# Performance work log

Hardware: AMD Instinct MI355X
Metric: run time of the kernel (lower is better)

The kernel has to match this reference:

```python
import jax, jax.numpy as jnp
import numpy as np
from jax import lax

B, CIN, H, W = 16, 96, 112, 112
C1, C2 = CIN * 2, CIN * 4          # 192, 384 (t1=(2,2))
SQ = 24                            # make_divisible(96//4, 4)
EPS = 1e-5


def _conv(x, w, stride, pad, groups):
    return lax.conv_general_dilated(
        x, w, window_strides=stride, padding=pad,
        feature_group_count=groups,
        dimension_numbers=("NCHW", "OIHW", "NCHW"))


def _bn(x, g, b, m, v):
    scale = (g / jnp.sqrt(v + EPS))[None, :, None, None]
    return (x - m[None, :, None, None]) * scale + b[None, :, None, None]


def _shuffle(x, groups):
    b, c, h, w = x.shape
    return x.reshape(b, groups, c // groups, h, w).transpose(0, 2, 1, 3, 4).reshape(b, c, h, w)


# DYShiftMax channel permutation for g=1: rotate channels left by 1
_DY_IDX = np.roll(np.arange(CIN), -1)


def setup_inputs() -> dict:
    key = jax.random.key(0)
    ks = jax.random.split(key, 16)
    f32 = jnp.float32
    d = {}
    d["x"] = jax.random.normal(ks[0], (B, CIN, H, W), f32)
    # depthwise (k,1) conv, groups=CIN, multiplier 2
    d["w_dw1"] = jax.random.normal(ks[1], (C1, 1, 3, 1), f32) * 0.2
    d["bn1_g"] = jax.random.uniform(ks[2], (C1,), f32, 0.5, 1.5)
    d["bn1_b"] = jax.random.normal(ks[3], (C1,), f32) * 0.1
    d["bn1_m"] = jax.random.normal(ks[4], (C1,), f32) * 0.1
    d["bn1_v"] = jax.random.uniform(ks[5], (C1,), f32, 0.5, 1.5)
    # depthwise (1,k) conv, groups=C1, multiplier 2
    d["w_dw2"] = jax.random.normal(ks[6], (C2, 1, 1, 3), f32) * 0.2
    d["bn2_g"] = jax.random.uniform(ks[7], (C2,), f32, 0.5, 1.5)
    d["bn2_b"] = jax.random.normal(ks[8], (C2,), f32) * 0.1
    d["bn2_m"] = jax.random.normal(ks[9], (C2,), f32) * 0.1
    d["bn2_v"] = jax.random.uniform(ks[10], (C2,), f32, 0.5, 1.5)
    # 1x1 pointwise conv 384 -> 96 (ConvModule, bias-free conv + BN, identity act)
    d["w_pw"] = jax.random.normal(ks[11], (CIN, C2, 1, 1), f32) * (1.0 / np.sqrt(C2))
    d["bn3_g"] = jax.random.uniform(ks[12], (CIN,), f32, 0.5, 1.5)
    d["bn3_b"] = jax.random.normal(ks[13], (CIN,), f32) * 0.1
    d["bn3_m"] = jax.random.normal(ks[14], (CIN,), f32) * 0.1
    d["bn3_v"] = jax.random.uniform(ks[15], (CIN,), f32, 0.5, 1.5)
    # DYShiftMax squeeze-excite FC: CIN -> SQ -> 2*CIN (exp=2)
    k2 = jax.random.split(jax.random.fold_in(key, 1), 4)
    d["fc1_w"] = jax.random.normal(k2[0], (SQ, CIN), f32) * (1.0 / np.sqrt(CIN))
    d["fc1_b"] = jax.random.normal(k2[1], (SQ,), f32) * 0.1
    d["fc2_w"] = jax.random.normal(k2[2], (2 * CIN, SQ), f32) * (1.0 / np.sqrt(SQ))
    d["fc2_b"] = jax.random.normal(k2[3], (2 * CIN,), f32) * 0.1
    return d


def reference(x, w_dw1, bn1_g, bn1_b, bn1_m, bn1_v,
              w_dw2, bn2_g, bn2_b, bn2_m, bn2_v,
              w_pw, bn3_g, bn3_b, bn3_m, bn3_v,
              fc1_w, fc1_b, fc2_w, fc2_b):
    # DepthSpatialSepConv: depthwise (3,1) then depthwise (1,3), each + BN
    h = _conv(x, w_dw1, (1, 1), ((1, 1), (0, 0)), groups=CIN)
    h = _bn(h, bn1_g, bn1_b, bn1_m, bn1_v)
    h = _conv(h, w_dw2, (1, 1), ((0, 0), (1, 1)), groups=C1)
    h = _bn(h, bn2_g, bn2_b, bn2_m, bn2_v)
    # ReLU6 (y2 == 0)
    h = jnp.clip(h, 0.0, 6.0)
    # ChannelShuffle(6)
    h = _shuffle(h, 6)
    # 1x1 ConvModule (groups=1, identity activation) + BN
    h = _conv(h, w_pw, (1, 1), ((0, 0), (0, 0)), groups=1)
    h = _bn(h, bn3_g, bn3_b, bn3_m, bn3_v)
    # DYShiftMax(out, out, (1,0), (0,0), act_relu=False -> exp=2, g=1)
    y = h.mean(axis=(2, 3))                       # [B, CIN] global avg pool
    y = jnp.maximum(y @ fc1_w.T + fc1_b, 0.0)     # Linear + ReLU
    y = y @ fc2_w.T + fc2_b                       # Linear -> [B, 2*CIN]
    y = jnp.clip(y + 3.0, 0.0, 6.0) / 6.0         # HSigmoid
    y = (y - 0.5) * 4.0
    a1 = y[:, :CIN] + 1.0                         # init_a[0] = 1.0
    b1 = y[:, CIN:]                               # init_b[0] = 0.0
    h2 = h[:, _DY_IDX, :, :]                      # shifted channels
    h = h * a1[:, :, None, None] + h2 * b1[:, :, None, None]
    # ChannelShuffle(g2=1) is identity; ChannelShuffle(out//2)
    h = _shuffle(h, CIN // 2)
    # residual (stride==1 and in==out)
    return h + x
```

## Files before the change

### kernel.cpp

```cpp
#include <hip/hip_runtime.h>
#include <hip/hip_bf16.h>

#define BATCH 16
#define CINC 96
#define HGT 112
#define WID 112
#define HW 12544
#define C1N 192
#define C2N 384
#define EPSV 1e-5f

typedef _Float16 f16x8 __attribute__((ext_vector_type(8)));
typedef _Float16 f16x4 __attribute__((ext_vector_type(4)));
typedef float    f32x4 __attribute__((ext_vector_type(4)));

#define WS_S      0
#define WS_A1B1   1536
#define WS_W1F    4608
#define WS_B1F    5184
#define WS_W2F    5376
#define WS_B2F    6528
#define WS_S3     6912
#define WS_B3     7008
#define WS_WPF_BYTES (7104*4)
#define WS_H_BYTES   (WS_WPF_BYTES + CINC*C2N*2)

__global__ void k_prep(const float* __restrict__ wdw1, const float* __restrict__ g1,
                       const float* __restrict__ bb1, const float* __restrict__ m1,
                       const float* __restrict__ v1,
                       const float* __restrict__ wdw2, const float* __restrict__ g2,
                       const float* __restrict__ bb2, const float* __restrict__ m2,
                       const float* __restrict__ v2,
                       const float* __restrict__ wpw, const float* __restrict__ g3,
                       const float* __restrict__ bb3, const float* __restrict__ m3,
                       const float* __restrict__ v3,
                       float* ws)
{
    int t = blockIdx.x * blockDim.x + threadIdx.x;
    int stride = gridDim.x * blockDim.x;
    float* w1f = ws + WS_W1F; float* b1f = ws + WS_B1F;
    float* w2f = ws + WS_W2F; float* b2f = ws + WS_B2F;
    float* s3  = ws + WS_S3;  float* b3f = ws + WS_B3;
    _Float16* wpf = (_Float16*)((char*)ws + WS_WPF_BYTES);

    for (int c = t; c < C1N; c += stride) {
        float s = g1[c] / sqrtf(v1[c] + EPSV);
        w1f[c*3+0] = wdw1[c*3+0] * s;
        w1f[c*3+1] = wdw1[c*3+1] * s;
        w1f[c*3+2] = wdw1[c*3+2] * s;
        b1f[c] = bb1[c] - m1[c] * s;
    }
    for (int c = t; c < C2N; c += stride) {
        float s = g2[c] / sqrtf(v2[c] + EPSV);
        w2f[c*3+0] = wdw2[c*3+0] * s;
        w2f[c*3+1] = wdw2[c*3+1] * s;
        w2f[c*3+2] = wdw2[c*3+2] * s;
        b2f[c] = bb2[c] - m2[c] * s;
    }
    for (int c = t; c < CINC; c += stride) {
        float s = g3[c] / sqrtf(v3[c] + EPSV);
        s3[c] = s; b3f[c] = bb3[c] - m3[c] * s;
    }
    for (int idx = t; idx < CINC * C2N; idx += stride) {
        int e = idx & 7;
        int l2 = idx >> 3;
        int lane = l2 & 63;
        int l3 = l2 >> 6;
        int rt = l3 % 6, ksg = l3 / 6;
        int m = rt * 16 + (lane & 15);
        int k = ksg * 32 + (lane >> 4) * 8 + e;
        int o = (k & 63) * 6 + (k >> 6);
        wpf[idx] = (_Float16)wpw[m * C2N + o];
    }
}

__global__ __launch_bounds__(256, 3) void k_main6(const float* __restrict__ x,
                                                  const float* __restrict__ ws,
                                                  float* __restrict__ sums,
                                                  _Float16* __restrict__ h_out)
{
    __shared__ __align__(16) char u_raw[256 * 208];
    __shared__ float ssum[CINC];

    int t   = threadIdx.x;
    int bid = blockIdx.x;
    int logical = (bid & 7) * 112 + (bid >> 3);
    int b   = logical / 56;
    int rem = logical - b * 56;
    int y0  = (rem >> 1) * 4;
    int x0  = (rem & 1) * 48;

    int wv = t >> 6, lane = t & 63;
    int r = lane >> 4, c4 = lane & 15;
    int gy = y0 + r;
    int gc = x0 + 4 * c4;
    int col16 = c4, g = r;

    const float* w1f = ws + WS_W1F; const float* b1f = ws + WS_B1F;
    const float* w2f = ws + WS_W2F; const float* b2f = ws + WS_B2F;

    if (t < CINC) ssum[t] = 0.f;

    bool ymok = gy >= 1;
    bool ypok = gy + 1 < HGT;
    bool isE  = (c4 == 0) | (c4 == 15);
    int  ecol = (c4 == 0) ? (x0 - 1) : (x0 + 64);
    bool ev   = isE && ((unsigned)ecol < (unsigned)WID);
    int  secol = ev ? ecol : 0;
    int  tm = ymok ? -WID : 0;
    int  tp = ypok ?  WID : 0;

    f32x4 acc[6][4];
    #pragma unroll
    for (int rt = 0; rt < 6; ++rt)
        #pragma unroll
        for (int ct = 0; ct < 4; ++ct) acc[rt][ct] = (f32x4){0.f, 0.f, 0.f, 0.f};

    const f16x8* wpf_g = (const f16x8*)((const char*)ws + WS_WPF_BYTES);
    long xb = (long)b * CINC * HW;
    long rowoff = (long)gy * WID;

    int rotbase = 3 * r + c4;
    char* ub0 = u_raw + (r * 64 + 4 * c4) * 208;

    for (int chunk = 0; chunk < 4; ++chunk) {
        if (chunk) __syncthreads();

        f16x4 uvbuf[4];
        #pragma unroll
        for (int i = 0; i < 6; ++i) {
            int cl = wv * 6 + i;
            int cu = __builtin_amdgcn_readfirstlane(chunk * 24 + cl);
            const float* xc = x + xb + (long)cu * HW;
            const float* xp = xc + rowoff + gc;
            f32x4 mid = *(const f32x4*)xp;
            f32x4 top = *(const f32x4*)(xp + tm);
            f32x4 bot = *(const f32x4*)(xp + tp);

            float eT = 0.f, eM = 0.f, eB = 0.f;
            if (isE) {
                const float* ep = xc + rowoff + secol;
                eM = ep[0];
                eT = ep[tm];
                eB = ep[tp];
            }

            int c1a = cu * 2;
            float wa0 = w1f[c1a*3+0], wa1 = w1f[c1a*3+1], wa2 = w1f[c1a*3+2], ba = b1f[c1a];
            float wb0 = w1f[c1a*3+3], wb1 = w1f[c1a*3+4], wb2 = w1f[c1a*3+5], bb = b1f[c1a+1];

            float va[4], vb[4];
            #pragma unroll
            for (int j = 0; j < 4; ++j) {
                float tt = ymok ? top[j] : 0.f;
                float bt = ypok ? bot[j] : 0.f;
                va[j] = fmaf(wa0, tt, fmaf(wa1, mid[j], fmaf(wa2, bt, ba)));
                vb[j] = fmaf(wb0, tt, fmaf(wb1, mid[j], fmaf(wb2, bt, bb)));
            }
            float etS = (ymok && ev) ? eT : 0.f;
            float ebS = (ypok && ev) ? eB : 0.f;
            float emS = ev ? eM : 0.f;
            float vea = ev ? fmaf(wa0, etS, fmaf(wa1, emS, fmaf(wa2, ebS, ba))) : 0.f;
            float veb = ev ? fmaf(wb0, etS, fmaf(wb1, emS, fmaf(wb2, ebS, bb))) : 0.f;

            float vLa = __shfl(va[3], (lane + 63) & 63);
            float vLb = __shfl(vb[3], (lane + 63) & 63);
            float vRa = __shfl(va[0], (lane + 1) & 63);
            float vRb = __shfl(vb[0], (lane + 1) & 63);
            if (c4 == 0)  { vLa = vea; vLb = veb; }
            if (c4 == 15) { vRa = vea; vRb = veb; }

            int c2b = cu * 4;
            float w20[4], w21[4], w22[4], b2v[4];
            #pragma unroll
            for (int jj = 0; jj < 4; ++jj) {
                w20[jj] = w2f[(c2b+jj)*3+0];
                w21[jj] = w2f[(c2b+jj)*3+1];
                w22[jj] = w2f[(c2b+jj)*3+2];
                b2v[jj] = b2f[c2b+jj];
            }

            float pa[6] = {vLa, va[0], va[1], va[2], va[3], vRa};
            float pb[6] = {vLb, vb[0], vb[1], vb[2], vb[3], vRb};

            f16x4 uv[4];
            #pragma unroll
            for (int j = 0; j < 4; ++j) {
                #pragma unroll
                for (int jj = 0; jj < 4; ++jj) {
                    float p0 = (jj < 2) ? pa[j]     : pb[j];
                    float p1 = (jj < 2) ? pa[j + 1] : pb[j + 1];
                    float p2 = (jj < 2) ? pa[j + 2] : pb[j + 2];
                    float tv = fmaf(w20[jj], p0, fmaf(w21[jj], p1, fmaf(w22[jj], p2, b2v[jj])));
                    tv = fminf(fmaxf(tv, 0.f), 6.f);
                    uv[j][jj] = (_Float16)tv;
                }
            }

            if ((i & 1) == 0) {
                #pragma unroll
                for (int j = 0; j < 4; ++j) uvbuf[j] = uv[j];
            } else {
                int slot = ((cl >> 1) + rotbase) % 12;
                char* ubase = ub0 + slot * 16;
                #pragma unroll
                for (int j = 0; j < 4; ++j) {
                    f16x8 w = __builtin_shufflevector(uvbuf[j], uv[j], 0, 1, 2, 3, 4, 5, 6, 7);
                    *(f16x8*)(ubase + j * 208) = w;
                }
            }
        }
        __syncthreads();

        #pragma unroll
        for (int ks = 0; ks < 3; ++ks) {
            f16x8 bfr[4];
            #pragma unroll
            for (int ct = 0; ct < 4; ++ct) {
                int pos = wv * 64 + ct * 16 + col16;
                int sl = (ks * 4 + g + 3 * wv + ((pos >> 2) & 15)) % 12;
                bfr[ct] = *(const f16x8*)(u_raw + pos * 208 + sl * 16);
            }
            #pragma unroll
            for (int rt = 0; rt < 6; ++rt) {
                f16x8 afr = wpf_g[((chunk * 3 + ks) * 6 + rt) * 64 + lane];
                #pragma unroll
                for (int ct = 0; ct < 4; ++ct)
                    acc[rt][ct] = __builtin_amdgcn_mfma_f32_16x16x32_f16(afr, bfr[ct], acc[rt][ct], 0, 0, 0);
            }
        }
    }
    __syncthreads();

    _Float16* h_s = (_Float16*)u_raw;
    const float* s3  = ws + WS_S3;
    const float* b3f = ws + WS_B3;
    #pragma unroll
    for (int rt = 0; rt < 6; ++rt) {
        #pragma unroll
        for (int ct = 0; ct < 4; ++ct) {
            int p = wv * 64 + ct * 16 + col16;
            #pragma unroll
            for (int rr = 0; rr < 4; ++rr) {
                int m = rt * 16 + g * 4 + rr;
                h_s[m * 264 + p] = (_Float16)fmaf(acc[rt][ct][rr], s3[m], b3f[m]);
            }
        }
    }
    __syncthreads();

    #pragma unroll
    for (int i = 0; i < 12; ++i) {
        int flat = i * 2048 + t * 8;
        int m = flat >> 8;
        int p = flat & 255;
        f16x8 hv = *(const f16x8*)(h_s + m * 264 + p);
        int row = y0 + (p >> 6);
        int colg = x0 + (p & 63);
        *(f16x8*)(h_out + ((long)(b * CINC + m)) * HW + (long)row * WID + colg) = hv;

        float s = 0.f;
        if (!(x0 == 48 && (p & 63) < 16)) {
            #pragma unroll
            for (int e = 0; e < 8; ++e) s += (float)hv[e];
        }
        s += __shfl_xor(s, 1);
        s += __shfl_xor(s, 2);
        s += __shfl_xor(s, 4);
        s += __shfl_xor(s, 8);
        s += __shfl_xor(s, 16);
        if ((lane & 31) == 0) atomicAdd(&ssum[m], s);
    }
    __syncthreads();
    if (t < CINC) atomicAdd(&sums[b * CINC + t], ssum[t]);
}

__global__ __launch_bounds__(192) void k_gates(const float* __restrict__ sums,
                                               const float* __restrict__ fc1w,
                                               const float* __restrict__ fc1b,
                                               const float* __restrict__ fc2w,
                                               const float* __restrict__ fc2b,
                                               float* __restrict__ a1b1)
{
    __shared__ float mean_s[CINC];
    __shared__ float mid[24];
    int b = blockIdx.x;
    int t = threadIdx.x;

    if (t < CINC) mean_s[t] = sums[b * CINC + t] * (1.0f / 12544.0f);
    __syncthreads();
    if (t < 24) {
        float d = fc1b[t];
        #pragma unroll 4
        for (int c = 0; c < CINC; ++c) d = fmaf(fc1w[t * CINC + c], mean_s[c], d);
        mid[t] = fmaxf(d, 0.f);
    }
    __syncthreads();
    {
        float d = fc2b[t];
        #pragma unroll
        for (int j = 0; j < 24; ++j) d = fmaf(fc2w[t * 24 + j], mid[j], d);
        float y = fminf(fmaxf(d + 3.f, 0.f), 6.f) * (1.f / 6.f);
        y = (y - 0.5f) * 4.f;
        a1b1[b * 192 + t] = (t < CINC) ? (y + 1.f) : y;
    }
}

__global__ __launch_bounds__(256) void k_final(const _Float16* __restrict__ h,
                                               const float* __restrict__ xin,
                                               const float* __restrict__ a1b1,
                                               float* __restrict__ out)
{
    int q = blockIdx.x * 256 + threadIdx.x;
    int pos4 = q % 3136;
    int bo = q / 3136;
    int o = bo % CINC, b = bo / CINC;
    int c = (o % 48) * 2 + (o / 48);
    int cn = (c + 1) % CINC;

    float av = a1b1[b * 192 + c];
    float bv = a1b1[b * 192 + 96 + c];

    long hb = (long)b * CINC * HW;
    f16x4 hv4 = *(const f16x4*)(h + hb + (long)c  * HW + pos4 * 4);
    f16x4 h2v = *(const f16x4*)(h + hb + (long)cn * HW + pos4 * 4);

    long xo = ((long)(b * CINC + o)) * HW + pos4 * 4;
    f32x4 xv = *(const f32x4*)(xin + xo);
    f32x4 rr;
    #pragma unroll
    for (int j = 0; j < 4; ++j)
        rr[j] = fmaf((float)hv4[j], av, fmaf((float)h2v[j], bv, xv[j]));
    *(f32x4*)(out + xo) = rr;
}

extern "C" void kernel_launch(void* const* d_in, const int* in_sizes, int n_in,
                              void* d_out, int out_size, void* d_ws, size_t ws_size,
                              hipStream_t stream)
{
    const float* x    = (const float*)d_in[0];
    const float* wdw1 = (const float*)d_in[1];
    const float* g1   = (const float*)d_in[2];
    const float* b1   = (const float*)d_in[3];
    const float* m1   = (const float*)d_in[4];
    const float* v1   = (const float*)d_in[5];
    const float* wdw2 = (const float*)d_in[6];
    const float* g2   = (const float*)d_in[7];
    const float* b2   = (const float*)d_in[8];
    const float* m2   = (const float*)d_in[9];
    const float* v2   = (const float*)d_in[10];
    const float* wpw  = (const float*)d_in[11];
    const float* g3   = (const float*)d_in[12];
    const float* b3   = (const float*)d_in[13];
    const float* m3   = (const float*)d_in[14];
    const float* v3   = (const float*)d_in[15];
    const float* fc1w = (const float*)d_in[16];
    const float* fc1b = (const float*)d_in[17];
    const float* fc2w = (const float*)d_in[18];
    const float* fc2b = (const float*)d_in[19];

    float* ws   = (float*)d_ws;
    float* sums = ws + WS_S;
    float* a1b1 = ws + WS_A1B1;
    _Float16* hbuf = (_Float16*)((char*)d_ws + WS_H_BYTES);
    float* out  = (float*)d_out;

    hipMemsetAsync(sums, 0, 1536 * sizeof(float), stream);
    k_prep<<<dim3(40), dim3(256), 0, stream>>>(
        wdw1, g1, b1, m1, v1, wdw2, g2, b2, m2, v2,
        wpw, g3, b3, m3, v3, ws);
    k_main6<<<dim3(896), dim3(256), 0, stream>>>(x, ws, sums, hbuf);
    k_gates<<<dim3(BATCH), dim3(192), 0, stream>>>(sums, fc1w, fc1b, fc2w, fc2b, a1b1);
    k_final<<<dim3(4816896 / 256), dim3(256), 0, stream>>>(hbuf, x, a1b1, out);
}
```

Measured before the change: 134.5 us.

## Software-pipeline input loads and stage pointwise weights through shared memory

Restructures the main fused kernel so input rows for channel pairs are loaded one pair ahead of the depthwise compute (double-buffered in registers). The pointwise-conv weight fragments for the next chunk are prefetched into registers and written to LDS, replacing per-MFMA global loads. Launch bounds drop from 3 to 2 blocks per SM to allow the extra register pressure, which reduces occupancy.

```diff
diff --git a/kernel.cpp b/kernel.cpp
--- a/kernel.cpp
+++ b/kernel.cpp
@@ -74,12 +74,18 @@
     }
 }
 
-__global__ __launch_bounds__(256, 3) void k_main6(const float* __restrict__ x,
+struct PairX {
+    f32x4 T[2], M[2], B[2];
+    float eT[2], eM[2], eB[2];
+};
+
+__global__ __launch_bounds__(256, 2) void k_main8(const float* __restrict__ x,
                                                   const float* __restrict__ ws,
                                                   float* __restrict__ sums,
                                                   _Float16* __restrict__ h_out)
 {
     __shared__ __align__(16) char u_raw[256 * 208];
+    __shared__ __align__(16) f16x8 wpf_s[1152];
     __shared__ float ssum[CINC];
 
     int t   = threadIdx.x;
@@ -118,97 +124,110 @@
 
     const f16x8* wpf_g = (const f16x8*)((const char*)ws + WS_WPF_BYTES);
     long xb = (long)b * CINC * HW;
-    long rowoff = (long)gy * WID;
+    const float* xw = x + xb + (long)gy * WID;
 
     int rotbase = 3 * r + c4;
     char* ub0 = u_raw + (r * 64 + 4 * c4) * 208;
 
+    f16x8 nw0 = wpf_g[t];
+    f16x8 nw1 = wpf_g[256 + t];
+    f16x8 nw2 = wpf_g[512 + t];
+    f16x8 nw3 = wpf_g[768 + t];
+    f16x8 nw4 = nw0;
+    if (t < 128) nw4 = wpf_g[1024 + t];
+
+    #define LOADCH(dst, q, cuq) {                                         \
+        const float* p_ = xw + (long)(cuq) * HW;                          \
+        (dst).M[q] = *(const f32x4*)(p_ + gc);                            \
+        (dst).T[q] = *(const f32x4*)(p_ + gc + tm);                       \
+        (dst).B[q] = *(const f32x4*)(p_ + gc + tp);                       \
+        if (isE) {                                                        \
+            const float* e_ = p_ + secol;                                 \
+            (dst).eM[q] = e_[0]; (dst).eT[q] = e_[tm]; (dst).eB[q] = e_[tp]; \
+        } }
+
     for (int chunk = 0; chunk < 4; ++chunk) {
         if (chunk) __syncthreads();
 
-        f16x4 uvbuf[4];
-        #pragma unroll
-        for (int i = 0; i < 6; ++i) {
-            int cl = wv * 6 + i;
-            int cu = __builtin_amdgcn_readfirstlane(chunk * 24 + cl);
-            const float* xc = x + xb + (long)cu * HW;
-            const float* xp = xc + rowoff + gc;
-            f32x4 mid = *(const f32x4*)xp;
-            f32x4 top = *(const f32x4*)(xp + tm);
-            f32x4 bot = *(const f32x4*)(xp + tp);
-
-            float eT = 0.f, eM = 0.f, eB = 0.f;
-            if (isE) {
-                const float* ep = xc + rowoff + secol;
-                eM = ep[0];
-                eT = ep[tm];
-                eB = ep[tp];
-            }
-
-            int c1a = cu * 2;
-            float wa0 = w1f[c1a*3+0], wa1 = w1f[c1a*3+1], wa2 = w1f[c1a*3+2], ba = b1f[c1a];
-            float wb0 = w1f[c1a*3+3], wb1 = w1f[c1a*3+4], wb2 = w1f[c1a*3+5], bb = b1f[c1a+1];
-
-            float va[4], vb[4];
-            #pragma unroll
-            for (int j = 0; j < 4; ++j) {
-                float tt = ymok ? top[j] : 0.f;
-                float bt = ypok ? bot[j] : 0.f;
-                va[j] = fmaf(wa0, tt, fmaf(wa1, mid[j], fmaf(wa2, bt, ba)));
-                vb[j] = fmaf(wb0, tt, fmaf(wb1, mid[j], fmaf(wb2, bt, bb)));
-            }
-            float etS = (ymok && ev) ? eT : 0.f;
-            float ebS = (ypok && ev) ? eB : 0.f;
-            float emS = ev ? eM : 0.f;
-            float vea = ev ? fmaf(wa0, etS, fmaf(wa1, emS, fmaf(wa2, ebS, ba))) : 0.f;
-            float veb = ev ? fmaf(wb0, etS, fmaf(wb1, emS, fmaf(wb2, ebS, bb))) : 0.f;
-
-            float vLa = __shfl(va[3], (lane + 63) & 63);
-            float vLb = __shfl(vb[3], (lane + 63) & 63);
-            float vRa = __shfl(va[0], (lane + 1) & 63);
-            float vRb = __shfl(vb[0], (lane + 1) & 63);
-            if (c4 == 0)  { vLa = vea; vLb = veb; }
-            if (c4 == 15) { vRa = vea; vRb = veb; }
-
-            int c2b = cu * 4;
-            float w20[4], w21[4], w22[4], b2v[4];
-            #pragma unroll
-            for (int jj = 0; jj < 4; ++jj) {
-                w20[jj] = w2f[(c2b+jj)*3+0];
-                w21[jj] = w2f[(c2b+jj)*3+1];
-                w22[jj] = w2f[(c2b+jj)*3+2];
-                b2v[jj] = b2f[c2b+jj];
-            }
-
-            float pa[6] = {vLa, va[0], va[1], va[2], va[3], vRa};
-            float pb[6] = {vLb, vb[0], vb[1], vb[2], vb[3], vRb};
-
-            f16x4 uv[4];
-            #pragma unroll
-            for (int j = 0; j < 4; ++j) {
-                #pragma unroll
-                for (int jj = 0; jj < 4; ++jj) {
-                    float p0 = (jj < 2) ? pa[j]     : pb[j];
-                    float p1 = (jj < 2) ? pa[j + 1] : pb[j + 1];
-                    float p2 = (jj < 2) ? pa[j + 2] : pb[j + 2];
-                    float tv = fmaf(w20[jj], p0, fmaf(w21[jj], p1, fmaf(w22[jj], p2, b2v[jj])));
-                    tv = fminf(fmaxf(tv, 0.f), 6.f);
-                    uv[j][jj] = (_Float16)tv;
-                }
-            }
-
-            if ((i & 1) == 0) {
-                #pragma unroll
-                for (int j = 0; j < 4; ++j) uvbuf[j] = uv[j];
-            } else {
-                int slot = ((cl >> 1) + rotbase) % 12;
-                char* ubase = ub0 + slot * 16;
+        wpf_s[t] = nw0;
+        wpf_s[256 + t] = nw1;
+        wpf_s[512 + t] = nw2;
+        wpf_s[768 + t] = nw3;
+        if (t < 128) wpf_s[1024 + t] = nw4;
+
+        int cbase = chunk * 24 + wv * 6;
+        PairX A, B;
+        LOADCH(A, 0, cbase + 0)
+        LOADCH(A, 1, cbase + 1)
+
+        #pragma unroll
+        for (int p = 0; p < 3; ++p) {
+            if (p == 0) { LOADCH(B, 0, cbase + 2) LOADCH(B, 1, cbase + 3) }
+            if (p == 1) { LOADCH(A, 0, cbase + 4) LOADCH(A, 1, cbase + 5) }
+            PairX& C = (p == 1) ? B : A;
+
+            f16x4 uv[2][4];
+            #pragma unroll
+            for (int q = 0; q < 2; ++q) {
+                int cu = cbase + 2 * p + q;
+                int c1a = cu * 2;
+                float wa0 = w1f[c1a*3+0], wa1 = w1f[c1a*3+1], wa2 = w1f[c1a*3+2], ba = b1f[c1a];
+                float wb0 = w1f[c1a*3+3], wb1 = w1f[c1a*3+4], wb2 = w1f[c1a*3+5], bb = b1f[c1a+1];
+
+                float va[4], vb[4];
                 #pragma unroll
                 for (int j = 0; j < 4; ++j) {
-                    f16x8 w = __builtin_shufflevector(uvbuf[j], uv[j], 0, 1, 2, 3, 4, 5, 6, 7);
-                    *(f16x8*)(ubase + j * 208) = w;
+                    float tt = ymok ? C.T[q][j] : 0.f;
+                    float bt = ypok ? C.B[q][j] : 0.f;
+                    va[j] = fmaf(wa0, tt, fmaf(wa1, C.M[q][j], fmaf(wa2, bt, ba)));
+                    vb[j] = fmaf(wb0, tt, fmaf(wb1, C.M[q][j], fmaf(wb2, bt, bb)));
                 }
-            }
+                float etS = (ymok && ev) ? C.eT[q] : 0.f;
+                float ebS = (ypok && ev) ? C.eB[q] : 0.f;
+                float emS = ev ? C.eM[q] : 0.f;
+                float vea = ev ? fmaf(wa0, etS, fmaf(wa1, emS, fmaf(wa2, ebS, ba))) : 0.f;
+                float veb = ev ? fmaf(wb0, etS, fmaf(wb1, emS, fmaf(wb2, ebS, bb))) : 0.f;
+
+                float vLa = __shfl(va[3], (lane + 63) & 63);
+                float vLb = __shfl(vb[3], (lane + 63) & 63);
+                float vRa = __shfl(va[0], (lane + 1) & 63);
+                float vRb = __shfl(vb[0], (lane + 1) & 63);
+                if (c4 == 0)  { vLa = vea; vLb = veb; }
+                if (c4 == 15) { vRa = vea; vRb = veb; }
+
+                int c2b = cu * 4;
+                float pa[6] = {vLa, va[0], va[1], va[2], va[3], vRa};
+                float pb[6] = {vLb, vb[0], vb[1], vb[2], vb[3], vRb};
+                #pragma unroll
+                for (int j = 0; j < 4; ++j) {
+                    #pragma unroll
+                    for (int jj = 0; jj < 4; ++jj) {
+                        float p0 = (jj < 2) ? pa[j]     : pb[j];
+                        float p1 = (jj < 2) ? pa[j + 1] : pb[j + 1];
+                        float p2 = (jj < 2) ? pa[j + 2] : pb[j + 2];
+                        float tv = fmaf(w2f[(c2b+jj)*3+0], p0,
+                                   fmaf(w2f[(c2b+jj)*3+1], p1,
+                                   fmaf(w2f[(c2b+jj)*3+2], p2, b2f[c2b+jj])));
+                        uv[q][j][jj] = (_Float16)fminf(fmaxf(tv, 0.f), 6.f);
+                    }
+                }
+            }
+            int slot = (wv * 3 + p + rotbase) % 12;
+            char* ubase = ub0 + slot * 16;
+            #pragma unroll
+            for (int j = 0; j < 4; ++j) {
+                f16x8 w = __builtin_shufflevector(uv[0][j], uv[1][j], 0, 1, 2, 3, 4, 5, 6, 7);
+                *(f16x8*)(ubase + j * 208) = w;
+            }
+        }
+
+        if (chunk < 3) {
+            int cb = (chunk + 1) * 1152;
+            nw0 = wpf_g[cb + t];
+            nw1 = wpf_g[cb + 256 + t];
+            nw2 = wpf_g[cb + 512 + t];
+            nw3 = wpf_g[cb + 768 + t];
+            if (t < 128) nw4 = wpf_g[cb + 1024 + t];
         }
         __syncthreads();
 
@@ -223,7 +242,7 @@
             }
             #pragma unroll
             for (int rt = 0; rt < 6; ++rt) {
-                f16x8 afr = wpf_g[((chunk * 3 + ks) * 6 + rt) * 64 + lane];
+                f16x8 afr = wpf_s[(ks * 6 + rt) * 64 + lane];
                 #pragma unroll
                 for (int ct = 0; ct < 4; ++ct)
                     acc[rt][ct] = __builtin_amdgcn_mfma_f32_16x16x32_f16(afr, bfr[ct], acc[rt][ct], 0, 0, 0);
@@ -369,7 +388,7 @@
     k_prep<<<dim3(40), dim3(256), 0, stream>>>(
         wdw1, g1, b1, m1, v1, wdw2, g2, b2, m2, v2,
         wpw, g3, b3, m3, v3, ws);
-    k_main6<<<dim3(896), dim3(256), 0, stream>>>(x, ws, sums, hbuf);
+    k_main8<<<dim3(896), dim3(256), 0, stream>>>(x, ws, sums, hbuf);
     k_gates<<<dim3(BATCH), dim3(192), 0, stream>>>(sums, fc1w, fc1b, fc2w, fc2b, a1b1);
     k_final<<<dim3(4816896 / 256), dim3(256), 0, stream>>>(hbuf, x, a1b1, out);
 }
```

Result: faster. 119.2 us (-11.4%).
